# Kernel optimization log

Hardware: AMD Instinct MI355X
Metric: run time of the kernel (lower is better)

Reference implementation:

```python
import jax, jax.numpy as jnp
import numpy as np

DIM = 1024
NUM_HEADS = 16
DIM_HEAD = 64
INNER = NUM_HEADS * DIM_HEAD  # 1024
B, N = 2, 2048


def setup_inputs() -> dict:
    key = jax.random.key(0)
    k1, k2, k3 = jax.random.split(key, 3)
    x = jax.random.normal(k1, (B, N, DIM), dtype=jnp.float32)
    # nn.Linear(dim, inner*3, bias=False): weight [3*inner, dim]; y = x @ W^T
    w_qkv = jax.random.normal(k2, (3 * INNER, DIM), dtype=jnp.float32) * (DIM ** -0.5)
    # to_out: Linear(inner, dim) with bias
    w_out = jax.random.normal(k3, (DIM, INNER), dtype=jnp.float32) * (INNER ** -0.5)
    b_out = jnp.zeros((DIM,), dtype=jnp.float32)
    return {"x": x, "w_qkv": w_qkv, "w_out": w_out, "b_out": b_out}


def reference(x, w_qkv, w_out, b_out):
    b, n, d = x.shape
    scale = DIM_HEAD ** -0.5
    qkv = jnp.einsum('bnd,ed->bne', x, w_qkv)  # [b, n, 3*inner]
    q, k, v = jnp.split(qkv, 3, axis=-1)
    # [b, n, h, dh] -> [b, h, n, dh]
    reshape = lambda t: t.reshape(b, n, NUM_HEADS, DIM_HEAD).transpose(0, 2, 1, 3)
    q, k, v = reshape(q), reshape(k), reshape(v)
    dots = jnp.einsum('bhqd,bhkd->bhqk', q, k) * scale  # [b, h, n, n]
    attn = jax.nn.softmax(dots, axis=-1)
    out = jnp.einsum('bhqk,bhkd->bhqd', attn, v)
    out = out.transpose(0, 2, 1, 3).reshape(b, n, INNER)
    out = jnp.einsum('bni,oi->bno', out, w_out) + b_out
    return out
```

## Files before the change

kernel.cpp:

```cpp
#include <hip/hip_runtime.h>
#include <hip/hip_bf16.h>
#include <stdint.h>

typedef unsigned short u16;
typedef short bf16x8 __attribute__((ext_vector_type(8)));
typedef float f32x4 __attribute__((ext_vector_type(4)));
typedef float f32x16 __attribute__((ext_vector_type(16)));
typedef u16 u16x4 __attribute__((ext_vector_type(4)));
typedef unsigned int uint2v __attribute__((ext_vector_type(2)));

#define DIMX  1024
#define NHEAD 16
#define DH    64
#define INNER 1024
#define BATCH 2
#define SEQ   2048
#define MTOT  (BATCH*SEQ)
#define EQKV  (3*INNER)
#define HSTRIDE 131072
#define TSTRIDE 4096

__device__ __forceinline__ u16 f2bf(float f) {
  unsigned int x = __float_as_uint(f);
  unsigned int r = (x + 0x7FFFu + ((x >> 16) & 1u)) >> 16;
  return (u16)r;
}

__device__ __forceinline__ unsigned int cvtpk(float lo, float hi) {
  unsigned int r;
  asm("v_cvt_pk_bf16_f32 %0, %1, %2" : "=v"(r) : "v"(lo), "v"(hi));
  return r;
}

__device__ __forceinline__ void plswap_u(unsigned int& x, unsigned int& y) {
  auto r = __builtin_amdgcn_permlane32_swap(x, y, false, false);
  x = r[0]; y = r[1];
}
__device__ __forceinline__ void plswap_f2(float v, float& a, float& b) {
  unsigned int x = __float_as_uint(v), y = __float_as_uint(v);
  auto r = __builtin_amdgcn_permlane32_swap(x, y, false, false);
  a = __uint_as_float(r[0]); b = __uint_as_float(r[1]);
}

__device__ __forceinline__ void async16(void* lds, const void* g) {
  __builtin_amdgcn_global_load_lds(
      (const __attribute__((address_space(1))) unsigned int*)g,
      (__attribute__((address_space(3))) unsigned int*)lds,
      16, 0, 0);
}

__device__ __forceinline__ int swz4(int r) { return (r ^ (r >> 2)) & 3; }

#define X4C (MTOT * DIMX / 4)
#define W4C (EQKV * DIMX / 4)
#define O4C (DIMX * INNER / 4)
__global__ void cvt_all(const float* __restrict__ x, const float* __restrict__ wq,
                        const float* __restrict__ wo, u16* __restrict__ xb,
                        u16* __restrict__ wqb, u16* __restrict__ wob) {
  int i = blockIdx.x * blockDim.x + threadIdx.x;
  const float* src; u16* dst; int off;
  if (i < X4C)            { src = x;  dst = xb;  off = i; }
  else if (i < X4C + W4C) { src = wq; dst = wqb; off = i - X4C; }
  else                    { src = wo; dst = wob; off = i - X4C - W4C; }
  float4 v = ((const float4*)src)[off];
  u16x4 o;
  o[0] = f2bf(v.x); o[1] = f2bf(v.y); o[2] = f2bf(v.z); o[3] = f2bf(v.w);
  ((u16x4*)dst)[off] = o;
}

__global__ __launch_bounds__(256) void gemm_qkv(const u16* __restrict__ X, const u16* __restrict__ W,
                                                u16* __restrict__ Qo, u16* __restrict__ Ko,
                                                u16* __restrict__ Vt) {
  __shared__ short sAll[24576];
  short* sA = sAll;
  short* sB = sAll + 12288;
  const int tid = threadIdx.x;
  const int wv = tid >> 6, l = tid & 63;
  const int lo = l & 15, hi = l >> 4;
  const int wr = wv >> 1, wc = wv & 1;

  int lin = blockIdx.x;
  int wgid = (lin & 7) * 96 + (lin >> 3);
  const int bx = wgid / 32;
  const int by = wgid % 32;
  const int tn = bx * 128, tm = by * 128;

  f32x4 acc[4][4];
#pragma unroll
  for (int i = 0; i < 4; i++)
#pragma unroll
    for (int j = 0; j < 4; j++) acc[i][j] = (f32x4){0.f, 0.f, 0.f, 0.f};

  auto stageT = [&](int buf, int kt) {
    int k0 = kt * 32;
    int off = buf * 4096;
#pragma unroll
    for (int c = 0; c < 2; c++) {
      int R0 = wv * 32 + c * 16;
      int r = R0 + (l >> 2);
      int sc = ((l & 3) ^ swz4(r)) * 8;
      async16(&sA[off + R0 * 32], &X[(size_t)(tm + r) * DIMX + k0 + sc]);
      async16(&sB[off + R0 * 32], &W[(size_t)(tn + r) * DIMX + k0 + sc]);
    }
  };

  auto compute = [&](int buf) {
    bf16x8 af[4], bf[4];
#pragma unroll
    for (int i = 0; i < 4; i++) {
      int r = wr * 64 + i * 16 + lo;
      af[i] = *(const bf16x8*)&sA[buf * 4096 + r * 32 + ((hi ^ swz4(r)) * 8)];
    }
#pragma unroll
    for (int j = 0; j < 4; j++) {
      int r = wc * 64 + j * 16 + lo;
      bf[j] = *(const bf16x8*)&sB[buf * 4096 + r * 32 + ((hi ^ swz4(r)) * 8)];
    }
#pragma unroll
    for (int i = 0; i < 4; i++)
#pragma unroll
      for (int j = 0; j < 4; j++)
        acc[i][j] = __builtin_amdgcn_mfma_f32_16x16x32_bf16(af[i], bf[j], acc[i][j], 0, 0, 0);
  };

  const int NT = DIMX / 32;
  stageT(0, 0);
  stageT(1, 1);
  int bc = 0;
  for (int kt = 0; kt < NT - 2; kt++) {
    int bs = bc + 2; if (bs >= 3) bs -= 3;
    stageT(bs, kt + 2);
    asm volatile("s_waitcnt vmcnt(8)" ::: "memory");
    asm volatile("s_barrier" ::: "memory");
    __builtin_amdgcn_sched_barrier(0);
    compute(bc);
    __builtin_amdgcn_sched_barrier(0);
    asm volatile("s_barrier" ::: "memory");
    bc = (bc == 2) ? 0 : bc + 1;
  }
  asm volatile("s_waitcnt vmcnt(4)" ::: "memory");
  asm volatile("s_barrier" ::: "memory");
  __builtin_amdgcn_sched_barrier(0);
  compute(bc);
  __builtin_amdgcn_sched_barrier(0);
  asm volatile("s_barrier" ::: "memory");
  bc = (bc == 2) ? 0 : bc + 1;
  asm volatile("s_waitcnt vmcnt(0)" ::: "memory");
  asm volatile("s_barrier" ::: "memory");
  __builtin_amdgcn_sched_barrier(0);
  compute(bc);
  __builtin_amdgcn_sched_barrier(0);
  __syncthreads();

  const int cls = tn >> 10;
  const float scale = 0.125f * 1.44269504088896f;

  if (cls == 0) {
#pragma unroll
    for (int i = 0; i < 4; i++) {
      int mbase = tm + wr * 64 + i * 16 + hi * 4;
#pragma unroll
      for (int j = 0; j < 4; j++) {
        int e = tn + wc * 64 + j * 16 + lo;
        int h = e >> 6, d = e & 63;
        size_t a0 = (((size_t)((mbase >> 11) * NHEAD + h)) * SEQ) * DH + d;
#pragma unroll
        for (int rp = 0; rp < 2; rp++) {
          int n0 = (mbase + rp * 2) & 2047;
          unsigned int pk = cvtpk(acc[i][j][rp * 2] * scale, acc[i][j][rp * 2 + 1] * scale);
          Qo[a0 + (size_t)n0 * DH] = (u16)pk;
          Qo[a0 + (size_t)(n0 + 1) * DH] = (u16)(pk >> 16);
        }
      }
    }
  } else if (cls == 1) {
#pragma unroll
    for (int i = 0; i < 4; i++) {
      int mbase = tm + wr * 64 + i * 16 + hi * 4;
      int b = mbase >> 11;
#pragma unroll
      for (int j = 0; j < 4; j++) {
        int e2 = (tn + wc * 64 + j * 16 + lo) - 1024;
        int h = e2 >> 6, d = e2 & 63;
        int kd = d >> 4, hi5k = (d >> 3) & 1, e8 = d & 7;
        size_t hb = (size_t)(b * NHEAD + h) * HSTRIDE + (size_t)kd * 512 + hi5k * 256 + e8;
#pragma unroll
        for (int rp = 0; rp < 2; rp++) {
          int n0 = (mbase + rp * 2) & 2047;
          int t_ = n0 >> 6, kvi = n0 & 63;
          int c = kvi >> 5, l31k = kvi & 31;
          unsigned int pk = cvtpk(acc[i][j][rp * 2], acc[i][j][rp * 2 + 1]);
          size_t a = hb + (size_t)t_ * TSTRIDE + c * 2048 + l31k * 8;
          Ko[a] = (u16)pk;
          Ko[a + 8] = (u16)(pk >> 16);
        }
      }
    }
  } else {
#pragma unroll
    for (int i = 0; i < 4; i++) {
#pragma unroll
      for (int j = 0; j < 4; j++) {
        int e = wc * 64 + j * 16 + lo;
#pragma unroll
        for (int rp = 0; rp < 2; rp++) {
          int n = wr * 64 + i * 16 + hi * 4 + rp * 2;
          unsigned int pk = cvtpk(acc[i][j][rp * 2], acc[i][j][rp * 2 + 1]);
          *(unsigned int*)&sAll[e * 128 + (((n >> 3) ^ (e & 15)) * 8) + (n & 7)] = pk;
        }
      }
    }
    __syncthreads();
    int er = tid >> 1, half = tid & 1;
    int e2 = tn + er - 2048;
    int h = e2 >> 6, dv = e2 & 63;
    int b = tm >> 11, nb = tm & 2047;
    int c = dv >> 5, l31v = dv & 31;
    size_t vb = (size_t)(b * NHEAD + h) * HSTRIDE
              + (size_t)((nb >> 6) + half) * TSTRIDE + (size_t)c * 2048 + l31v * 8;
#pragma unroll
    for (int k = 0; k < 8; k++) {
      int phys = (half * 8 + k) ^ (er & 15);
      bf16x8 v = *(const bf16x8*)&sAll[er * 128 + phys * 8];
      int ks = k >> 1, hi5v = k & 1;
      *(bf16x8*)&Vt[vb + ks * 512 + hi5v * 256] = v;
    }
  }
}

__global__ __launch_bounds__(256) void attn_kernel(const u16* __restrict__ Q, const u16* __restrict__ Ksh,
                                                   const u16* __restrict__ Vsh, u16* __restrict__ O) {
  const int tid = threadIdx.x, wv = tid >> 6, l = tid & 63;
  const int l31 = l & 31, hi5 = l >> 5;

  int lin = blockIdx.y * gridDim.x + blockIdx.x;
  int wgid = (lin & 7) * 64 + (lin >> 3);
  int bx = wgid & 15;
  int bh = wgid >> 4;

  const int qw = bx * 128 + wv * 32;
  const u16* Qb = Q + (size_t)bh * SEQ * DH;
  const u16* Kb = Ksh + (size_t)bh * HSTRIDE + l * 8;
  const u16* Vb = Vsh + (size_t)bh * HSTRIDE + l * 8;

  bf16x8 qf[4];
#pragma unroll
  for (int kd = 0; kd < 4; kd++)
    qf[kd] = *(const bf16x8*)&Qb[(size_t)(qw + l31) * DH + kd * 16 + hi5 * 8];

  f32x16 o0, o1;
#pragma unroll
  for (int r = 0; r < 16; r++) { o0[r] = 0.f; o1[r] = 0.f; }
  float lsum = 0.f;
  const float CSHIFT = 12.0f;

  bf16x8 kA0[4], kA1[4], kB0[4], kB1[4];

  auto loadK = [&](bf16x8 (&k0)[4], bf16x8 (&k1)[4], int t) {
    const u16* p = Kb + (size_t)t * TSTRIDE;
#pragma unroll
    for (int kd = 0; kd < 4; kd++) {
      k0[kd] = *(const bf16x8*)&p[kd * 512];
      k1[kd] = *(const bf16x8*)&p[2048 + kd * 512];
    }
  };

  auto tile = [&](bf16x8 (&kc0)[4], bf16x8 (&kc1)[4],
                  bf16x8 (&kn0)[4], bf16x8 (&kn1)[4], int t) {
    const u16* pv = Vb + (size_t)t * TSTRIDE;
    bf16x8 vf0[4], vf1[4];
#pragma unroll
    for (int ks = 0; ks < 4; ks++) {
      vf0[ks] = *(const bf16x8*)&pv[ks * 512];
      vf1[ks] = *(const bf16x8*)&pv[2048 + ks * 512];
    }
    if (t + 1 < SEQ / 64) loadK(kn0, kn1, t + 1);

    f32x16 s0, s1;
#pragma unroll
    for (int r = 0; r < 16; r++) { s0[r] = -CSHIFT; s1[r] = -CSHIFT; }
#pragma unroll
    for (int kd = 0; kd < 4; kd++) {
      s0 = __builtin_amdgcn_mfma_f32_32x32x16_bf16(kc0[kd], qf[kd], s0, 0, 0, 0);
      s1 = __builtin_amdgcn_mfma_f32_32x32x16_bf16(kc1[kd], qf[kd], s1, 0, 0, 0);
    }

    float sm[16];
#pragma unroll
    for (int r = 0; r < 16; r++) {
      s0[r] = __builtin_amdgcn_exp2f(s0[r]);
      s1[r] = __builtin_amdgcn_exp2f(s1[r]);
      sm[r] = s0[r] + s1[r];
    }
#pragma unroll
    for (int st = 8; st > 0; st >>= 1)
#pragma unroll
      for (int r = 0; r < st; r++) sm[r] += sm[r + st];
    lsum += sm[0];

    bf16x8 pa[4];
#pragma unroll
    for (int ks = 0; ks < 4; ks++) {
      const int sft = (ks & 1) * 8;
      float e0 = (ks < 2) ? s0[sft + 0] : s1[sft + 0];
      float e1 = (ks < 2) ? s0[sft + 1] : s1[sft + 1];
      float e2 = (ks < 2) ? s0[sft + 2] : s1[sft + 2];
      float e3 = (ks < 2) ? s0[sft + 3] : s1[sft + 3];
      float e4 = (ks < 2) ? s0[sft + 4] : s1[sft + 4];
      float e5 = (ks < 2) ? s0[sft + 5] : s1[sft + 5];
      float e6 = (ks < 2) ? s0[sft + 6] : s1[sft + 6];
      float e7 = (ks < 2) ? s0[sft + 7] : s1[sft + 7];
      unsigned int w0 = cvtpk(e0, e1);
      unsigned int w1 = cvtpk(e2, e3);
      unsigned int w2 = cvtpk(e4, e5);
      unsigned int w3 = cvtpk(e6, e7);
      plswap_u(w0, w2);
      plswap_u(w1, w3);
      union { unsigned int w[4]; bf16x8 v; } u;
      u.w[0] = w0; u.w[1] = w1; u.w[2] = w2; u.w[3] = w3;
      pa[ks] = u.v;
    }

#pragma unroll
    for (int ks = 0; ks < 4; ks++) {
      o0 = __builtin_amdgcn_mfma_f32_32x32x16_bf16(vf0[ks], pa[ks], o0, 0, 0, 0);
      o1 = __builtin_amdgcn_mfma_f32_32x32x16_bf16(vf1[ks], pa[ks], o1, 0, 0, 0);
    }
  };

  loadK(kA0, kA1, 0);
  for (int t = 0; t < SEQ / 64; t += 2) {
    tile(kA0, kA1, kB0, kB1, t);
    tile(kB0, kB1, kA0, kA1, t + 1);
  }

  float la, lb;
  plswap_f2(lsum, la, lb);
  float inv = 1.0f / (la + lb);

  int b = bh >> 4, h = bh & 15;
  int q = qw + l31;
  size_t orow = ((size_t)(b * SEQ + q)) * INNER + h * 64;
#pragma unroll
  for (int half = 0; half < 2; half++) {
    const f32x16& oo = half ? o1 : o0;
#pragma unroll
    for (int g = 0; g < 4; g++) {
      uint2v pk2;
      pk2[0] = cvtpk(oo[g * 4 + 0] * inv, oo[g * 4 + 1] * inv);
      pk2[1] = cvtpk(oo[g * 4 + 2] * inv, oo[g * 4 + 3] * inv);
      int dv = half * 32 + g * 8 + 4 * hi5;
      *(uint2v*)&O[orow + dv] = pk2;
    }
  }
}

__global__ __launch_bounds__(256) void gemm_out(const u16* __restrict__ A, const u16* __restrict__ W,
                                                const float* __restrict__ bias, float* __restrict__ out) {
  __shared__ short sAll[12288];
  short* sA = sAll;
  short* sB = sAll + 8192;
  const int tid = threadIdx.x;
  const int wv = tid >> 6, l = tid & 63;
  const int lo = l & 15, hi = l >> 4;
  const int wr = wv >> 1, wc = wv & 1;

  int lin = blockIdx.x;
  int wgid = (lin & 7) * 64 + (lin >> 3);
  const int bx = wgid / 32;
  const int by = wgid % 32;
  const int tn = bx * 64, tm = by * 128;

  f32x4 acc[4][2];
#pragma unroll
  for (int i = 0; i < 4; i++)
#pragma unroll
    for (int j = 0; j < 2; j++) acc[i][j] = (f32x4){0.f, 0.f, 0.f, 0.f};

  auto stage = [&](int buf, int kt) {
    int k0 = kt * 32;
#pragma unroll
    for (int c = 0; c < 2; c++) {
      int R0 = wv * 32 + c * 16;
      int r = R0 + (l >> 2);
      int sc = ((l & 3) ^ swz4(r)) * 8;
      async16(&sA[buf * 4096 + R0 * 32], &A[(size_t)(tm + r) * INNER + k0 + sc]);
    }
    int rB = wv * 16 + (l >> 2);
    int scB = ((l & 3) ^ swz4(rB)) * 8;
    async16(&sB[buf * 2048 + (wv * 16) * 32], &W[(size_t)(tn + rB) * INNER + k0 + scB]);
  };

  stage(0, 0);
  __syncthreads();

  for (int kt = 0; kt < INNER / 32; kt++) {
    const int buf = kt & 1;
    if (kt + 1 < INNER / 32) stage(buf ^ 1, kt + 1);
    bf16x8 af[4], bf[2];
#pragma unroll
    for (int i = 0; i < 4; i++) {
      int r = wr * 64 + i * 16 + lo;
      af[i] = *(const bf16x8*)&sA[buf * 4096 + r * 32 + ((hi ^ swz4(r)) * 8)];
    }
#pragma unroll
    for (int j = 0; j < 2; j++) {
      int r = wc * 32 + j * 16 + lo;
      bf[j] = *(const bf16x8*)&sB[buf * 2048 + r * 32 + ((hi ^ swz4(r)) * 8)];
    }
#pragma unroll
    for (int i = 0; i < 4; i++)
#pragma unroll
      for (int j = 0; j < 2; j++)
        acc[i][j] = __builtin_amdgcn_mfma_f32_16x16x32_bf16(af[i], bf[j], acc[i][j], 0, 0, 0);
    __syncthreads();
  }

#pragma unroll
  for (int i = 0; i < 4; i++) {
    int mbase = tm + wr * 64 + i * 16 + hi * 4;
#pragma unroll
    for (int j = 0; j < 2; j++) {
      int col = tn + wc * 32 + j * 16 + lo;
      float bv = bias[col];
#pragma unroll
      for (int r = 0; r < 4; r++)
        out[(size_t)(mbase + r) * DIMX + col] = acc[i][j][r] + bv;
    }
  }
}

extern "C" void kernel_launch(void* const* d_in, const int* in_sizes, int n_in,
                              void* d_out, int out_size, void* d_ws, size_t ws_size,
                              hipStream_t stream) {
  const float* x     = (const float*)d_in[0];
  const float* w_qkv = (const float*)d_in[1];
  const float* w_out = (const float*)d_in[2];
  const float* b_out = (const float*)d_in[3];

  char* ws = (char*)d_ws;
  u16* xb    = (u16*)(ws);
  u16* wqkvb = (u16*)(ws + (size_t)8  * (1<<20));
  u16* woutb = (u16*)(ws + (size_t)14 * (1<<20));
  u16* Qd    = (u16*)(ws + (size_t)16 * (1<<20));
  u16* Kdd   = (u16*)(ws + (size_t)24 * (1<<20));
  u16* Vtd   = (u16*)(ws + (size_t)32 * (1<<20));
  u16* Od    = (u16*)(ws + (size_t)40 * (1<<20));

  cvt_all<<<(X4C + W4C + O4C) / 256, 256, 0, stream>>>(x, w_qkv, w_out, xb, wqkvb, woutb);

  gemm_qkv<<<768, 256, 0, stream>>>(xb, wqkvb, Qd, Kdd, Vtd);
  attn_kernel<<<dim3(SEQ / 128, BATCH * NHEAD), 256, 0, stream>>>(Qd, Kdd, Vtd, Od);
  gemm_out<<<512, 256, 0, stream>>>(Od, woutb, b_out, (float*)d_out);
}
```

Measured before the change: 115.9 us.

## Split attention over two KV halves and merge partials with log-sum-exp

The attention grid doubles, and each workgroup processes half of the key/value sequence. Each half writes a normalized bf16 partial output, stored transposed, plus a per-row log-sum-exp into workspace. A new merge kernel blends the two partials with a sigmoid of the LSE difference and writes the usual head-interleaved output. The aim is more parallelism and better CU fill in the attention stage. The cost is an extra kernel launch, partial-output traffic and some reduced precision from rounding the partials to bf16.

```diff
diff --git a/kernel.cpp b/kernel.cpp
--- a/kernel.cpp
+++ b/kernel.cpp
@@ -229,14 +229,18 @@
 }
 
 __global__ __launch_bounds__(256) void attn_kernel(const u16* __restrict__ Q, const u16* __restrict__ Ksh,
-                                                   const u16* __restrict__ Vsh, u16* __restrict__ O) {
+                                                   const u16* __restrict__ Vsh,
+                                                   u16* __restrict__ OpA, u16* __restrict__ OpB,
+                                                   float* __restrict__ LseA, float* __restrict__ LseB) {
   const int tid = threadIdx.x, wv = tid >> 6, l = tid & 63;
   const int l31 = l & 31, hi5 = l >> 5;
 
   int lin = blockIdx.y * gridDim.x + blockIdx.x;
-  int wgid = (lin & 7) * 64 + (lin >> 3);
-  int bx = wgid & 15;
-  int bh = wgid >> 4;
+  int wgid = (lin & 7) * 128 + (lin >> 3);
+  int bh = wgid >> 5;
+  int rest = wgid & 31;
+  int bx = rest >> 1;
+  int half = rest & 1;
 
   const int qw = bx * 128 + wv * 32;
   const u16* Qb = Q + (size_t)bh * SEQ * DH;
@@ -255,6 +259,7 @@
   const float CSHIFT = 12.0f;
 
   bf16x8 kA0[4], kA1[4], kB0[4], kB1[4];
+  const int t0 = half * 16, t1 = t0 + 16;
 
   auto loadK = [&](bf16x8 (&k0)[4], bf16x8 (&k1)[4], int t) {
     const u16* p = Kb + (size_t)t * TSTRIDE;
@@ -274,7 +279,7 @@
       vf0[ks] = *(const bf16x8*)&pv[ks * 512];
       vf1[ks] = *(const bf16x8*)&pv[2048 + ks * 512];
     }
-    if (t + 1 < SEQ / 64) loadK(kn0, kn1, t + 1);
+    if (t + 1 < t1) loadK(kn0, kn1, t + 1);
 
     f32x16 s0, s1;
 #pragma unroll
@@ -328,30 +333,68 @@
     }
   };
 
-  loadK(kA0, kA1, 0);
-  for (int t = 0; t < SEQ / 64; t += 2) {
+  loadK(kA0, kA1, t0);
+  for (int t = t0; t < t1; t += 2) {
     tile(kA0, kA1, kB0, kB1, t);
     tile(kB0, kB1, kA0, kA1, t + 1);
   }
 
   float la, lb;
   plswap_f2(lsum, la, lb);
-  float inv = 1.0f / (la + lb);
-
-  int b = bh >> 4, h = bh & 15;
+  float lt = la + lb;
+  float inv = 1.0f / lt;
+  float lse = CSHIFT + __log2f(lt);
+
+  u16* Op = half ? OpB : OpA;
+  float* Lse = half ? LseB : LseA;
   int q = qw + l31;
-  size_t orow = ((size_t)(b * SEQ + q)) * INNER + h * 64;
-#pragma unroll
-  for (int half = 0; half < 2; half++) {
-    const f32x16& oo = half ? o1 : o0;
-#pragma unroll
-    for (int g = 0; g < 4; g++) {
-      uint2v pk2;
-      pk2[0] = cvtpk(oo[g * 4 + 0] * inv, oo[g * 4 + 1] * inv);
-      pk2[1] = cvtpk(oo[g * 4 + 2] * inv, oo[g * 4 + 3] * inv);
-      int dv = half * 32 + g * 8 + 4 * hi5;
-      *(uint2v*)&O[orow + dv] = pk2;
-    }
+  if (hi5 == 0) Lse[(size_t)bh * SEQ + q] = lse;
+
+  u16* Obase = Op + (size_t)bh * DH * SEQ;
+#pragma unroll
+  for (int r = 0; r < 16; r++) {
+    int dv = (r & 3) + 8 * (r >> 2) + 4 * hi5;
+    Obase[(size_t)dv * SEQ + q] = f2bf(o0[r] * inv);
+    Obase[(size_t)(dv + 32) * SEQ + q] = f2bf(o1[r] * inv);
+  }
+}
+
+__global__ __launch_bounds__(256) void merge_kernel(const u16* __restrict__ OpA, const u16* __restrict__ OpB,
+                                                    const float* __restrict__ LseA, const float* __restrict__ LseB,
+                                                    u16* __restrict__ O) {
+  __shared__ float lsA[64 * 65];
+  __shared__ float lsB[64 * 65];
+  const int tid = threadIdx.x;
+  const int bh = blockIdx.y, qc = blockIdx.x;
+  const int b = bh >> 4, h = bh & 15;
+
+#pragma unroll
+  for (int i = 0; i < 2; i++) {
+    int idx = tid + i * 256;
+    int dv = idx >> 3, q8 = (idx & 7) * 8;
+    size_t goff = (size_t)bh * DH * SEQ + (size_t)dv * SEQ + qc * 64 + q8;
+    bf16x8 va = *(const bf16x8*)&OpA[goff];
+    bf16x8 vb = *(const bf16x8*)&OpB[goff];
+#pragma unroll
+    for (int j = 0; j < 8; j++) {
+      lsA[dv * 65 + q8 + j] = __uint_as_float(((unsigned int)(u16)va[j]) << 16);
+      lsB[dv * 65 + q8 + j] = __uint_as_float(((unsigned int)(u16)vb[j]) << 16);
+    }
+  }
+  __syncthreads();
+
+  const int lane = tid & 63, w = tid >> 6;
+#pragma unroll
+  for (int i = 0; i < 16; i++) {
+    int ql = w * 16 + i;
+    int q = qc * 64 + ql;
+    float la = LseA[(size_t)bh * SEQ + q];
+    float lb = LseB[(size_t)bh * SEQ + q];
+    float sig = 1.0f / (1.0f + __builtin_amdgcn_exp2f(lb - la));
+    float va = lsA[lane * 65 + ql];
+    float vb = lsB[lane * 65 + ql];
+    float out = vb + (va - vb) * sig;
+    O[((size_t)(b * SEQ + q)) * INNER + h * 64 + lane] = f2bf(out);
   }
 }
 
@@ -446,10 +489,15 @@
   u16* Kdd   = (u16*)(ws + (size_t)24 * (1<<20));
   u16* Vtd   = (u16*)(ws + (size_t)32 * (1<<20));
   u16* Od    = (u16*)(ws + (size_t)40 * (1<<20));
+  u16*   OpA  = (u16*)(ws);
+  u16*   OpB  = (u16*)(ws + (size_t)48 * (1<<20));
+  float* LseA = (float*)(ws + (size_t)8 * (1<<20));
+  float* LseB = (float*)(ws + (size_t)8 * (1<<20) + (1<<19));
 
   cvt_all<<<(X4C + W4C + O4C) / 256, 256, 0, stream>>>(x, w_qkv, w_out, xb, wqkvb, woutb);
 
   gemm_qkv<<<768, 256, 0, stream>>>(xb, wqkvb, Qd, Kdd, Vtd);
-  attn_kernel<<<dim3(SEQ / 128, BATCH * NHEAD), 256, 0, stream>>>(Qd, Kdd, Vtd, Od);
+  attn_kernel<<<dim3(SEQ / 128 * 2, BATCH * NHEAD), 256, 0, stream>>>(Qd, Kdd, Vtd, OpA, OpB, LseA, LseB);
+  merge_kernel<<<dim3(SEQ / 64, BATCH * NHEAD), 256, 0, stream>>>(OpA, OpB, LseA, LseB, Od);
   gemm_out<<<512, 256, 0, stream>>>(Od, woutb, b_out, (float*)d_out);
 }
```

After: 129.1 us. 11.3% more time.
